# Kernel tuning notes

Hardware: AMD Instinct MI355X
Metric: run time of the kernel (lower is better)

The kernel has to match this reference:

```python
import jax, jax.numpy as jnp
import numpy as np

N_HEAD = 8
D_HEAD = 128   # dim_k = dim_q = dim_v
SEG_LEN = 512
EPS = 1e-6


def setup_inputs() -> dict:
    key = jax.random.key(0)
    ks = jax.random.split(key, 8)
    B, T, D = 2, 4096, 1024
    scale = 0.02
    x = jax.random.normal(ks[0], (B, T, D), dtype=jnp.float32)
    w_q = jax.random.normal(ks[1], (D, N_HEAD * D_HEAD), dtype=jnp.float32) * scale
    w_k = jax.random.normal(ks[2], (D, N_HEAD * D_HEAD), dtype=jnp.float32) * scale
    w_v = jax.random.normal(ks[3], (D, N_HEAD * D_HEAD), dtype=jnp.float32) * scale
    b_q = jnp.zeros((N_HEAD * D_HEAD,), jnp.float32)
    b_k = jnp.zeros((N_HEAD * D_HEAD,), jnp.float32)
    b_v = jnp.zeros((N_HEAD * D_HEAD,), jnp.float32)
    beta = jnp.zeros((N_HEAD,), jnp.float32)
    return {"x": x, "w_q": w_q, "b_q": b_q, "w_k": w_k, "b_k": b_k,
            "w_v": w_v, "b_v": b_v, "beta": beta}


def _heads(y, B, T):
    # [B,T,H*D] -> [B,H,T,D]
    return y.reshape(B, T, N_HEAD, D_HEAD).transpose(0, 2, 1, 3)


def reference(x, w_q, b_q, w_k, b_k, w_v, b_v, beta):
    B, T, _ = x.shape
    S = T // SEG_LEN
    q = _heads(x @ w_q + b_q, B, T)
    k = _heads(x @ w_k + b_k, B, T)
    v = _heads(x @ w_v + b_v, B, T)

    # segment: [B,H,T,D] -> [S,B,H,L,D]
    def seg(y):
        return y.reshape(B, N_HEAD, S, SEG_LEN, D_HEAD).transpose(2, 0, 1, 3, 4)
    qs, ks_, vs = seg(q), seg(k), seg(v)

    causal = jnp.tril(jnp.ones((SEG_LEN, SEG_LEN), bool))
    gate = jax.nn.sigmoid(beta).reshape(1, N_HEAD, 1, 1)
    inv_sqrt_d = 1.0 / jnp.sqrt(jnp.asarray(D_HEAD, x.dtype))

    def step(carry, segdat):
        M, z = carry                      # M: [B,H,Dk,Dv], z: [B,H,Dk]
        qc, kc, vc = segdat               # [B,H,L,D]
        sq = jax.nn.elu(qc) + 1.0
        sk = jax.nn.elu(kc) + 1.0
        # retrieval from memory BEFORE update
        a_mem = jnp.einsum('bhld,bhde->bhle', sq, M) / (
            jnp.einsum('bhld,bhd->bhl', sq, z)[..., None] + EPS)
        # delta-rule memory update
        retr_k = jnp.einsum('bhld,bhde->bhle', sk, M) / (
            jnp.einsum('bhld,bhd->bhl', sk, z)[..., None] + EPS)
        M = M + jnp.einsum('bhld,bhle->bhde', sk, vc - retr_k)
        z = z + sk.sum(axis=2)
        # local causal dot-product attention within the segment
        scores = jnp.einsum('bhld,bhmd->bhlm', qc, kc) * inv_sqrt_d
        scores = jnp.where(causal, scores, jnp.asarray(-1e30, scores.dtype))
        a_dot = jnp.einsum('bhlm,bhmd->bhld', jax.nn.softmax(scores, axis=-1), vc)
        # long-term context injection
        a = gate * a_mem + (1.0 - gate) * a_dot
        return (M, z), a

    M0 = jnp.zeros((B, N_HEAD, D_HEAD, D_HEAD), x.dtype)
    z0 = jnp.zeros((B, N_HEAD, D_HEAD), x.dtype)
    _, out = jax.lax.scan(step, (M0, z0), (qs, ks_, vs))
    # [S,B,H,L,D] -> [B,T,H*D]
    out = out.transpose(1, 3, 0, 2, 4).reshape(B, T, N_HEAD * D_HEAD)
    # wait: axes of out are [S,B,H,L,D]; reorder to [B,S,L,H,D]
    return out


# fix ordering: define reference properly (overrides above draft path)
def reference(x, w_q, b_q, w_k, b_k, w_v, b_v, beta):
    B, T, _ = x.shape
    S = T // SEG_LEN
    q = _heads(x @ w_q + b_q, B, T)
    k = _heads(x @ w_k + b_k, B, T)
    v = _heads(x @ w_v + b_v, B, T)

    def seg(y):
        return y.reshape(B, N_HEAD, S, SEG_LEN, D_HEAD).transpose(2, 0, 1, 3, 4)
    qs, ks_, vs = seg(q), seg(k), seg(v)

    causal = jnp.tril(jnp.ones((SEG_LEN, SEG_LEN), bool))
    gate = jax.nn.sigmoid(beta).reshape(1, N_HEAD, 1, 1)
    inv_sqrt_d = 1.0 / jnp.sqrt(jnp.asarray(D_HEAD, x.dtype))

    def step(carry, segdat):
        M, z = carry
        qc, kc, vc = segdat
        sq = jax.nn.elu(qc) + 1.0
        sk = jax.nn.elu(kc) + 1.0
        a_mem = jnp.einsum('bhld,bhde->bhle', sq, M) / (
            jnp.einsum('bhld,bhd->bhl', sq, z)[..., None] + EPS)
        retr_k = jnp.einsum('bhld,bhde->bhle', sk, M) / (
            jnp.einsum('bhld,bhd->bhl', sk, z)[..., None] + EPS)
        M = M + jnp.einsum('bhld,bhle->bhde', sk, vc - retr_k)
        z = z + sk.sum(axis=2)
        scores = jnp.einsum('bhld,bhmd->bhlm', qc, kc) * inv_sqrt_d
        scores = jnp.where(causal, scores, jnp.asarray(-1e30, scores.dtype))
        a_dot = jnp.einsum('bhlm,bhmd->bhld', jax.nn.softmax(scores, axis=-1), vc)
        a = gate * a_mem + (1.0 - gate) * a_dot
        return (M, z), a

    M0 = jnp.zeros((B, N_HEAD, D_HEAD, D_HEAD), x.dtype)
    z0 = jnp.zeros((B, N_HEAD, D_HEAD), x.dtype)
    _, out = jax.lax.scan(step, (M0, z0), (qs, ks_, vs))  # [S,B,H,L,D]
    out = out.transpose(1, 0, 3, 2, 4).reshape(B, T, N_HEAD * D_HEAD)
    return out
```

## Files before the change

### kernel.cpp

```cpp
#include <hip/hip_runtime.h>
#include <hip/hip_bf16.h>

typedef __attribute__((ext_vector_type(8))) short bf16x8;
typedef __attribute__((ext_vector_type(4))) float f32x4;
typedef unsigned short u16;
typedef unsigned int u32;

#define DEV static __device__ __forceinline__

DEV float bf2f(u16 u){ u32 x = ((u32)u)<<16; float f; __builtin_memcpy(&f,&x,4); return f; }
DEV u16 f2bf(float f){ u32 x; __builtin_memcpy(&x,&f,4); return (u16)((x + 0x7fffu + ((x>>16)&1u))>>16); }
DEV float elu1(float x){ return x > 0.f ? x + 1.f : __expf(x); }

DEV void gload16(const u16* g, u16* l){
  __builtin_amdgcn_global_load_lds(
      (const __attribute__((address_space(1))) unsigned int*)(g),
      (__attribute__((address_space(3))) unsigned int*)(l), 16, 0, 0);
}

#define MFMA(a,b,c) __builtin_amdgcn_mfma_f32_16x16x32_bf16((a),(b),(c),0,0,0)

#define NB 2
#define NT 4096
#define NH 8
#define DH 128
#define NS 8
#define SL 512
#define ND 1024
#define N3 3072
#define EPS 1e-6f

__global__ __launch_bounds__(256) void k_xc(const float* __restrict__ x, u16* __restrict__ xb){
  int i = blockIdx.x*256 + threadIdx.x;
  const float4 v0 = *(const float4*)(x + (size_t)i*8);
  const float4 v1 = *(const float4*)(x + (size_t)i*8 + 4);
  bf16x8 o;
  o[0]=(short)f2bf(v0.x); o[1]=(short)f2bf(v0.y); o[2]=(short)f2bf(v0.z); o[3]=(short)f2bf(v0.w);
  o[4]=(short)f2bf(v1.x); o[5]=(short)f2bf(v1.y); o[6]=(short)f2bf(v1.z); o[7]=(short)f2bf(v1.w);
  *(bf16x8*)(xb + (size_t)i*8) = o;
}

__global__ __launch_bounds__(256) void k_wt(const float* __restrict__ wq,
                                            const float* __restrict__ wk,
                                            const float* __restrict__ wv,
                                            u16* __restrict__ wt,
                                            float* __restrict__ cs){
  __shared__ float t[32][33];
  const int z = blockIdx.z;
  const float* w = (z==0) ? wq : (z==1 ? wk : wv);
  const int k0 = blockIdx.x*32, n0 = blockIdx.y*32;
  const int tx = threadIdx.x, ty = threadIdx.y;
  if (z==0 && blockIdx.x==0 && blockIdx.y==0){
    const int tid = ty*32 + tx;
#pragma unroll
    for (int i=0;i<64;i++) cs[tid + i*256] = 0.f;
  }
#pragma unroll
  for (int i=0;i<4;i++) t[ty+i*8][tx] = w[(size_t)(k0+ty+i*8)*ND + n0+tx];
  __syncthreads();
#pragma unroll
  for (int i=0;i<4;i++)
    wt[(size_t)(z*ND + n0+ty+i*8)*ND + k0+tx] = f2bf(t[tx][ty+i*8]);
}

__global__ __launch_bounds__(256) void k_gemm(const u16* __restrict__ xb,
                                              const u16* __restrict__ wt,
                                              const float* __restrict__ bq,
                                              const float* __restrict__ bk,
                                              const float* __restrict__ bv,
                                              u16* __restrict__ qkv){
  __shared__ __align__(16) u16 As[128*64];
  __shared__ __align__(16) u16 Bs[128*64];
  const int m0 = blockIdx.x*128, n0 = blockIdx.y*128;
  const int tid = threadIdx.x;
  const int w = tid>>6, lane = tid&63, g = lane>>4, li = lane&15;
  const int wr = w>>1, wc = w&1;
  const int srow = lane>>3;
  const int ssl  = (lane&7) ^ srow;
  f32x4 z4 = {0.f,0.f,0.f,0.f};
  f32x4 acc[4][4];
#pragma unroll
  for (int mi=0;mi<4;mi++)
#pragma unroll
    for (int ni=0;ni<4;ni++) acc[mi][ni] = z4;

  for (int kt=0; kt<16; ++kt){
    const int k0 = kt*64;
#pragma unroll
    for (int i=0;i<4;i++){
      const int c = i*4 + w;
      const int row = c*8 + srow;
      gload16(xb + (size_t)(m0+row)*ND + k0 + ssl*8, As + c*512);
      gload16(wt + (size_t)(n0+row)*ND + k0 + ssl*8, Bs + c*512);
    }
    __syncthreads();
#pragma unroll
    for (int kk=0;kk<2;kk++){
      bf16x8 a[4], bb[4];
#pragma unroll
      for (int mi=0;mi<4;mi++){
        int row = wr*64 + mi*16 + li;
        int slot = kk*4 + g;
        a[mi] = *(const bf16x8*)(As + row*64 + ((slot^(row&7))<<3));
      }
#pragma unroll
      for (int ni=0;ni<4;ni++){
        int row = wc*64 + ni*16 + li;
        int slot = kk*4 + g;
        bb[ni] = *(const bf16x8*)(Bs + row*64 + ((slot^(row&7))<<3));
      }
#pragma unroll
      for (int mi=0;mi<4;mi++)
#pragma unroll
        for (int ni=0;ni<4;ni++)
          acc[mi][ni] = MFMA(a[mi], bb[ni], acc[mi][ni]);
    }
    __syncthreads();
  }
#pragma unroll
  for (int ni=0;ni<4;ni++){
    int n = n0 + wc*64 + ni*16 + li;
    float bias = (n < ND) ? bq[n] : (n < 2*ND ? bk[n-ND] : bv[n-2*ND]);
#pragma unroll
    for (int mi=0;mi<4;mi++)
#pragma unroll
      for (int rr=0;rr<4;rr++){
        int m = m0 + wr*64 + mi*16 + 4*g + rr;
        qkv[(size_t)m*N3 + n] = f2bf(acc[mi][ni][rr] + bias);
      }
  }
}

__global__ __launch_bounds__(256) void k_tr(const u16* __restrict__ qkv,
                                            u16* __restrict__ vt,
                                            u16* __restrict__ pkT,
                                            float* __restrict__ cs){
  __shared__ __align__(4) u16 t[64*66];
  __shared__ float pf[8][64];
  const int t0 = blockIdx.x*64, d0 = blockIdx.y*64;
  const int z = blockIdx.z, bh = z>>1, part = z&1;
  const int b = bh>>3, h = bh&7;
  const int basec = (part ? 2*ND : ND) + h*DH;
  const int tid = threadIdx.x;
  float s0 = 0.f, s1 = 0.f;
#pragma unroll
  for (int i=0;i<8;i++){
    int fp = tid + i*256;
    int row = fp>>5, c2 = (fp&31)*2;
    ushort2 v = *(const ushort2*)(qkv + (size_t)(b*NT + t0+row)*N3 + basec + d0 + c2);
    if (!part){
      float e0 = elu1(bf2f(v.x)), e1 = elu1(bf2f(v.y));
      s0 += e0; s1 += e1;
      v.x = f2bf(e0); v.y = f2bf(e1);
    }
    *(ushort2*)(t + row*66 + c2) = v;
  }
  if (!part){ pf[tid>>5][(tid&31)*2] = s0; pf[tid>>5][(tid&31)*2+1] = s1; }
  __syncthreads();
  u16* dst = part ? vt : pkT;
#pragma unroll
  for (int i=0;i<8;i++){
    int fp = tid + i*256;
    int dr = fp>>5, c2 = (fp&31)*2;
    ushort2 v; v.x = t[c2*66 + dr]; v.y = t[(c2+1)*66 + dr];
    *(ushort2*)(dst + (size_t)(bh*DH + d0+dr)*NT + t0 + c2) = v;
  }
  if (!part && tid < 64){
    float a = 0.f;
#pragma unroll
    for (int r=0;r<8;r++) a += pf[r][tid];
    const int bhs = b*64 + h*8 + (t0>>9);
    atomicAdd(&cs[(size_t)bhs*DH + d0 + tid], a);
  }
}

__global__ __launch_bounds__(512) void k_dinv(const u16* __restrict__ qkv,
                                              const float* __restrict__ cs,
                                              float* __restrict__ dinvK){
  const int bhs = blockIdx.x, half = blockIdx.y;
  const int b = bhs>>6, h = (bhs>>3)&7, s = bhs&7;
  const int tid = threadIdx.x, w = tid>>6, lane = tid&63, grp = lane>>4, li = lane&15;
  __shared__ float zl[128];
  if (tid < 128){
    float a = 0.f;
    for (int sp=0; sp<s; ++sp) a += cs[(size_t)(bhs - s + sp)*DH + tid];
    zl[tid] = a;
  }
  __syncthreads();
#pragma unroll
  for (int it=0; it<8; ++it){
    const int r = half*256 + w*32 + it*4 + grp;
    bf16x8 v = *(const bf16x8*)(qkv + (size_t)(b*NT + s*SL + r)*N3 + ND + h*DH + li*8);
    float p = 0.f;
#pragma unroll
    for (int j=0;j<8;j++) p += elu1(bf2f((u16)v[j])) * zl[li*8+j];
    p += __shfl_xor(p,1); p += __shfl_xor(p,2);
    p += __shfl_xor(p,4); p += __shfl_xor(p,8);
    if (li == 0) dinvK[(size_t)bhs*SL + r] = 1.f/(p + EPS);
  }
}

__global__ __launch_bounds__(512) void k_gram(const u16* __restrict__ pkT,
                                              const u16* __restrict__ vtb,
                                              const float* __restrict__ dinvK,
                                              u16* __restrict__ G, float* __restrict__ Bm){
  const int bhs = blockIdx.x, ec = blockIdx.y;
  const int bh = bhs>>3, s = bhs&7, tb = s*SL;
  const int tid = threadIdx.x, w = tid>>6, lane = tid&63, g = lane>>4, li = lane&15;
  __shared__ __align__(16) u16 Bk[32*512];
  __shared__ __align__(16) u16 Bv[32*512];
  __shared__ float dv[512];
  dv[tid] = dinvK[(size_t)bhs*SL + tid];
#pragma unroll
  for (int i=0;i<4;i++){
    const int ee = i*8 + w;
    const size_t rowo = ((size_t)bh*DH + ec*32 + ee)*NT + tb + ((lane^w)<<3);
    gload16(pkT + rowo, Bk + ee*512);
    gload16(vtb + rowo, Bv + ee*512);
  }
  __syncthreads();
  f32x4 z4 = {0.f,0.f,0.f,0.f};
  f32x4 Ga[2] = {z4,z4}, Ba[2] = {z4,z4};
  const u16* arow = pkT + ((size_t)bh*DH + 16*w + li)*NT + tb;
  for (int ks=0; ks<16; ++ks){
    const int r0 = ks*32 + g*8;
    bf16x8 araw = *(const bf16x8*)(arow + r0);
    float4 d0 = *(const float4*)(dv + r0);
    float4 d1 = *(const float4*)(dv + r0 + 4);
    bf16x8 ascl;
    ascl[0] = (short)f2bf(bf2f((u16)araw[0]) * d0.x);
    ascl[1] = (short)f2bf(bf2f((u16)araw[1]) * d0.y);
    ascl[2] = (short)f2bf(bf2f((u16)araw[2]) * d0.z);
    ascl[3] = (short)f2bf(bf2f((u16)araw[3]) * d0.w);
    ascl[4] = (short)f2bf(bf2f((u16)araw[4]) * d1.x);
    ascl[5] = (short)f2bf(bf2f((u16)araw[5]) * d1.y);
    ascl[6] = (short)f2bf(bf2f((u16)araw[6]) * d1.z);
    ascl[7] = (short)f2bf(bf2f((u16)araw[7]) * d1.w);
    const int slot = ks*4 + g;
#pragma unroll
    for (int ni=0;ni<2;ni++){
      const int ee = ni*16 + li;
      bf16x8 bk8 = *(const bf16x8*)(Bk + ee*512 + ((slot^(li&7))<<3));
      bf16x8 bv8 = *(const bf16x8*)(Bv + ee*512 + ((slot^(li&7))<<3));
      Ga[ni] = MFMA(ascl, bk8, Ga[ni]);
      Ba[ni] = MFMA(araw, bv8, Ba[ni]);
    }
  }
#pragma unroll
  for (int ni=0;ni<2;ni++)
#pragma unroll
    for (int rr=0;rr<4;rr++){
      const int dd = 16*w + 4*g + rr;
      const int ee = ec*32 + ni*16 + li;
      G[((size_t)bhs*DH + dd)*DH + ee] = f2bf(Ga[ni][rr]);
      Bm[((size_t)bhs*DH + dd)*DH + ee] = Ba[ni][rr];
    }
}

__global__ __launch_bounds__(512) void k_scan(const u16* __restrict__ G,
                                              const float* __restrict__ Bm,
                                              u16* __restrict__ MTs){
  const int bh = blockIdx.x;
  const int tid = threadIdx.x, w = tid>>6, lane = tid&63, g = lane>>4, li = lane&15;
  __shared__ __align__(16) u16 MT[16384];
  for (int i = tid; i < 16384; i += 512) MT[i] = 0;
  __syncthreads();
  for (int s=0;s<NS;s++){
    const size_t bhs = (size_t)bh*NS + s;
    for (int f = tid; f < 2048; f += 512){
      int e = f>>4, sl = f&15;
      bf16x8 v = *(const bf16x8*)(MT + e*128 + ((sl^(e&7))<<3));
      *(bf16x8*)(MTs + bhs*16384 + e*128 + sl*8) = v;
    }
    __syncthreads();
    f32x4 z4 = {0.f,0.f,0.f,0.f};
    f32x4 acc[8];
#pragma unroll
    for (int i=0;i<8;i++) acc[i] = z4;
#pragma unroll
    for (int ks=0;ks<4;ks++){
      bf16x8 a = *(const bf16x8*)(G + (bhs*DH + 16*w + li)*DH + ks*32 + g*8);
#pragma unroll
      for (int ni=0;ni<8;ni++){
        int e = ni*16 + li;
        int sl = ks*4 + g;
        bf16x8 bfr = *(const bf16x8*)(MT + e*128 + ((sl^(e&7))<<3));
        acc[ni] = MFMA(a, bfr, acc[ni]);
      }
    }
    __syncthreads();
#pragma unroll
    for (int ni=0;ni<8;ni++)
#pragma unroll
      for (int rr=0;rr<4;rr++){
        int dd = 16*w + 4*g + rr, ee = ni*16 + li;
        float delta = Bm[(bhs*DH + dd)*DH + ee] - acc[ni][rr];
        int idx = ee*128 + (((dd>>3)^(ee&7))<<3) + (dd&7);
        MT[idx] = f2bf(bf2f(MT[idx]) + delta);
      }
    __syncthreads();
  }
}

__global__ __launch_bounds__(512) void k_attn(const u16* __restrict__ qkv,
                                              const u16* __restrict__ vtb,
                                              const u16* __restrict__ MTs,
                                              const float* __restrict__ cs,
                                              const float* __restrict__ beta,
                                              float* __restrict__ out){
  const int bhs = blockIdx.x, half = blockIdx.y;
  const int b = bhs>>6, h = (bhs>>3)&7, s = bhs&7, bh = bhs>>3;
  const int tid = threadIdx.x, w = tid>>6, lane = tid&63, g = lane>>4, li = lane&15;
  const int jq = (w < 4) ? (half + 2*w) : (15 - half - 2*(w-4));
  const int qb = jq*32;
  const float gate = 1.f/(1.f + __expf(-beta[h]));
  const float isd = 0.08838834764831845f;
  const float L2E = 1.4426950408889634f;
  __shared__ __align__(16) u16 P[8*1024];
  __shared__ float zl[128];
  __shared__ float dinvW[8][32];
  u16* Pw = P + w*1024;

  if (tid < 128){
    float a = 0.f;
    for (int sp=0; sp<s; ++sp) a += cs[(size_t)(bhs - s + sp)*DH + tid];
    zl[tid] = a;
  }
  __syncthreads();

  {
    const int r = qb + (lane&31);
    const int dh = (lane>>5)*64;
    const u16* qrow = qkv + (size_t)(b*NT + s*SL + r)*N3 + h*DH + dh;
    float p = 0.f;
#pragma unroll
    for (int j=0;j<64;j+=8){
      bf16x8 v = *(const bf16x8*)(qrow + j);
#pragma unroll
      for (int t=0;t<8;t++) p += elu1(bf2f((u16)v[t])) * zl[dh + j + t];
    }
    p += __shfl_xor(p, 32);
    if (lane < 32) dinvW[w][lane] = 1.f/(p + EPS);
  }

  bf16x8 qf[2][4];
#pragma unroll
  for (int mf=0; mf<2; ++mf)
#pragma unroll
    for (int kf=0; kf<4; ++kf)
      qf[mf][kf] = *(const bf16x8*)(qkv + (size_t)(b*NT + s*SL + qb + mf*16 + li)*N3 + h*DH + kf*32 + g*8);

  f32x4 z4 = {0.f,0.f,0.f,0.f};
  f32x4 O[2][8];
  float mr[2][4], lr[2][4];
#pragma unroll
  for (int mf=0;mf<2;++mf){
#pragma unroll
    for (int nf=0;nf<8;++nf) O[mf][nf] = z4;
#pragma unroll
    for (int rr=0;rr<4;++rr){ mr[mf][rr] = -3e38f; lr[mf][rr] = 0.f; }
  }

  const int nch = jq + 1;
  for (int c=0; c<nch; ++c){
    const int kb = c*32;
    f32x4 sa[2][2];
#pragma unroll
    for (int mf=0;mf<2;++mf)
#pragma unroll
      for (int nf=0;nf<2;++nf) sa[mf][nf] = z4;
#pragma unroll
    for (int kf=0; kf<4; ++kf)
#pragma unroll
      for (int nf=0; nf<2; ++nf){
        bf16x8 bk8 = *(const bf16x8*)(qkv + (size_t)(b*NT + s*SL + kb + nf*16 + li)*N3 + ND + h*DH + kf*32 + g*8);
        sa[0][nf] = MFMA(qf[0][kf], bk8, sa[0][nf]);
        sa[1][nf] = MFMA(qf[1][kf], bk8, sa[1][nf]);
      }
    float pv[2][2][4];
#pragma unroll
    for (int mf=0;mf<2;++mf)
#pragma unroll
      for (int nf=0;nf<2;++nf)
#pragma unroll
        for (int rr=0;rr<4;++rr){
          int row = qb + mf*16 + 4*g + rr, col = kb + nf*16 + li;
          float v = sa[mf][nf][rr]*isd;
          pv[mf][nf][rr] = (col > row) ? -1e30f : v;
        }
#pragma unroll
    for (int mf=0;mf<2;++mf)
#pragma unroll
      for (int rr=0;rr<4;++rr){
        float cm = fmaxf(pv[mf][0][rr], pv[mf][1][rr]);
        cm = fmaxf(cm, __shfl_xor(cm, 1));
        cm = fmaxf(cm, __shfl_xor(cm, 2));
        cm = fmaxf(cm, __shfl_xor(cm, 4));
        cm = fmaxf(cm, __shfl_xor(cm, 8));
        float mo = mr[mf][rr];
        float mn = fmaxf(mo, cm);
        float sc = exp2f((mo - mn)*L2E);
        float rs = 0.f;
#pragma unroll
        for (int nf=0;nf<2;++nf){
          float p = exp2f((pv[mf][nf][rr]-mn)*L2E);
          pv[mf][nf][rr] = p; rs += p;
        }
        rs += __shfl_xor(rs, 1); rs += __shfl_xor(rs, 2);
        rs += __shfl_xor(rs, 4); rs += __shfl_xor(rs, 8);
        lr[mf][rr] = lr[mf][rr]*sc + rs;
        mr[mf][rr] = mn;
#pragma unroll
        for (int nf=0;nf<8;++nf) O[mf][nf][rr] *= sc;
      }
#pragma unroll
    for (int mf=0;mf<2;++mf)
#pragma unroll
      for (int nf=0;nf<2;++nf)
#pragma unroll
        for (int rr=0;rr<4;++rr){
          int row = mf*16 + 4*g + rr, col = nf*16 + li;
          Pw[row*32 + (((col>>3)^(row&3))<<3) + (col&7)] = f2bf(pv[mf][nf][rr]);
        }
    bf16x8 pa[2];
#pragma unroll
    for (int mf=0;mf<2;++mf){
      int row = mf*16 + li;
      pa[mf] = *(const bf16x8*)(Pw + row*32 + ((g^(row&3))<<3));
    }
#pragma unroll
    for (int nf=0;nf<8;++nf){
      bf16x8 bv8 = *(const bf16x8*)(vtb + ((size_t)bh*DH + nf*16 + li)*NT + s*SL + kb + g*8);
      O[0][nf] = MFMA(pa[0], bv8, O[0][nf]);
      O[1][nf] = MFMA(pa[1], bv8, O[1][nf]);
    }
  }

  f32x4 Am[2][8];
#pragma unroll
  for (int mf=0;mf<2;++mf)
#pragma unroll
    for (int nf=0;nf<8;++nf) Am[mf][nf] = z4;
#pragma unroll
  for (int ks=0;ks<4;++ks){
    bf16x8 pq[2];
#pragma unroll
    for (int mf=0;mf<2;++mf){
      bf16x8 raw = *(const bf16x8*)(qkv + (size_t)(b*NT + s*SL + qb + mf*16 + li)*N3 + h*DH + ks*32 + g*8);
#pragma unroll
      for (int j=0;j<8;j++) raw[j] = (short)f2bf(elu1(bf2f((u16)raw[j])));
      pq[mf] = raw;
    }
#pragma unroll
    for (int nf=0;nf<8;++nf){
      bf16x8 bfr = *(const bf16x8*)(MTs + ((size_t)bhs*DH + nf*16 + li)*DH + ks*32 + g*8);
      Am[0][nf] = MFMA(pq[0], bfr, Am[0][nf]);
      Am[1][nf] = MFMA(pq[1], bfr, Am[1][nf]);
    }
  }

  const float og = 1.f - gate;
#pragma unroll
  for (int mf=0;mf<2;++mf)
#pragma unroll
    for (int rr=0;rr<4;++rr){
      int row = qb + mf*16 + 4*g + rr;
      float invd = og / lr[mf][rr];
      float dv = gate * dinvW[w][row - qb];
#pragma unroll
      for (int nf=0;nf<8;++nf)
        out[(size_t)(b*NT + s*SL + row)*ND + h*DH + nf*16 + li] =
            O[mf][nf][rr]*invd + Am[mf][nf][rr]*dv;
    }
}

extern "C" void kernel_launch(void* const* d_in, const int* in_sizes, int n_in,
                              void* d_out, int out_size, void* d_ws, size_t ws_size,
                              hipStream_t stream) {
  (void)in_sizes; (void)n_in; (void)out_size; (void)ws_size;
  const float* x    = (const float*)d_in[0];
  const float* wq   = (const float*)d_in[1];
  const float* bq   = (const float*)d_in[2];
  const float* wk   = (const float*)d_in[3];
  const float* bk   = (const float*)d_in[4];
  const float* wv   = (const float*)d_in[5];
  const float* bv   = (const float*)d_in[6];
  const float* beta = (const float*)d_in[7];
  float* out = (float*)d_out;
  char* ws = (char*)d_ws;

  u16*   wt  = (u16*)  (ws + 0);
  u16*   qkv = (u16*)  (ws + 6291456);
  u16*   vt  = (u16*)  (ws + 56623104);
  u16*   pkT = (u16*)  (ws + 73400320);
  u16*   G   = (u16*)  (ws + 90177536);
  float* Bm  = (float*)(ws + 94371840);
  u16*   MTs = (u16*)  (ws + 102760448);
  float* cs  = (float*)(ws + 106954752);
  u16*   xb  = vt;
  float* dinvK = (float*)(ws + 107020288);

  hipLaunchKernelGGL(k_xc,    dim3(4096),    dim3(256),  0, stream, x, xb);
  hipLaunchKernelGGL(k_wt,    dim3(32,32,3), dim3(32,8), 0, stream, wq, wk, wv, wt, cs);
  hipLaunchKernelGGL(k_gemm,  dim3(64,24),   dim3(256),  0, stream, xb, wt, bq, bk, bv, qkv);
  hipLaunchKernelGGL(k_tr,    dim3(64,2,32), dim3(256),  0, stream, qkv, vt, pkT, cs);
  hipLaunchKernelGGL(k_dinv,  dim3(128,2),   dim3(512),  0, stream, qkv, cs, dinvK);
  hipLaunchKernelGGL(k_gram,  dim3(128,4),   dim3(512),  0, stream, pkT, vt, dinvK, G, Bm);
  hipLaunchKernelGGL(k_scan,  dim3(16),      dim3(512),  0, stream, G, Bm, MTs);
  hipLaunchKernelGGL(k_attn,  dim3(128,2),   dim3(512),  0, stream, qkv, vt, MTs, cs, beta, out);
}
```

Baseline: 203.8 us.

## Double-buffer QKV GEMM with 256x256 tiles and phased async prefetch

Rewrites the bf16 QKV projection GEMM to use 256x256 block tiles with 512 threads and double-buffered LDS. The next k-tile is prefetched in four slices spread across four compute phases, with explicit vmcnt waits, barriers and raised MFMA issue priority. The goal is to hide global-to-LDS load latency behind MFMA work and to reuse each LDS tile more. In exchange, the 128KB LDS footprint allows only one block per CU, and 384 blocks on the CUs leave a partial second wave.

```diff
diff --git a/kernel.cpp b/kernel.cpp
--- a/kernel.cpp
+++ b/kernel.cpp
@@ -63,70 +63,116 @@
     wt[(size_t)(z*ND + n0+ty+i*8)*ND + k0+tx] = f2bf(t[tx][ty+i*8]);
 }
 
-__global__ __launch_bounds__(256) void k_gemm(const u16* __restrict__ xb,
+__global__ __launch_bounds__(512) void k_gemm(const u16* __restrict__ xb,
                                               const u16* __restrict__ wt,
                                               const float* __restrict__ bq,
                                               const float* __restrict__ bk,
                                               const float* __restrict__ bv,
                                               u16* __restrict__ qkv){
-  __shared__ __align__(16) u16 As[128*64];
-  __shared__ __align__(16) u16 Bs[128*64];
-  const int m0 = blockIdx.x*128, n0 = blockIdx.y*128;
-  const int tid = threadIdx.x;
-  const int w = tid>>6, lane = tid&63, g = lane>>4, li = lane&15;
-  const int wr = w>>1, wc = w&1;
+  __shared__ __align__(16) u16 As[2][256*64];
+  __shared__ __align__(16) u16 Bs[2][256*64];
+  const int tid = threadIdx.x, w = tid>>6, lane = tid&63, g = lane>>4, li = lane&15;
+  const int wr = w>>2, wc = w&3;
+  const int m0 = blockIdx.x*256, n0 = blockIdx.y*256;
   const int srow = lane>>3;
   const int ssl  = (lane&7) ^ srow;
+
   f32x4 z4 = {0.f,0.f,0.f,0.f};
-  f32x4 acc[4][4];
-#pragma unroll
-  for (int mi=0;mi<4;mi++)
-#pragma unroll
-    for (int ni=0;ni<4;ni++) acc[mi][ni] = z4;
-
-  for (int kt=0; kt<16; ++kt){
-    const int k0 = kt*64;
-#pragma unroll
-    for (int i=0;i<4;i++){
-      const int c = i*4 + w;
-      const int row = c*8 + srow;
-      gload16(xb + (size_t)(m0+row)*ND + k0 + ssl*8, As + c*512);
-      gload16(wt + (size_t)(n0+row)*ND + k0 + ssl*8, Bs + c*512);
-    }
-    __syncthreads();
-#pragma unroll
-    for (int kk=0;kk<2;kk++){
-      bf16x8 a[4], bb[4];
-#pragma unroll
-      for (int mi=0;mi<4;mi++){
-        int row = wr*64 + mi*16 + li;
-        int slot = kk*4 + g;
-        a[mi] = *(const bf16x8*)(As + row*64 + ((slot^(row&7))<<3));
+  f32x4 acc[8][4];
+#pragma unroll
+  for (int mi=0;mi<8;mi++)
+#pragma unroll
+    for (int nf=0;nf<4;nf++) acc[mi][nf] = z4;
+
+#define STG(t_, h_) do{                                                         \
+    u16* dst_ = ((h_)&1) ? (u16*)Bs[(t_)&1] : (u16*)As[(t_)&1];                 \
+    const u16* src_ = ((h_)&1) ? wt : xb;                                       \
+    const int o0_ = ((h_)&1) ? n0 : m0;                                         \
+    const int rb0_ = (((h_)>>1)<<7) + w*8;                                      \
+    _Pragma("unroll")                                                           \
+    for (int r_=0;r_<2;r_++){                                                   \
+      const int rb_ = rb0_ + r_*64;                                             \
+      gload16(src_ + (size_t)(o0_+rb_+srow)*ND + (t_)*64 + ssl*8, dst_ + rb_*64);\
+    }                                                                           \
+  }while(0)
+
+#define PHASE(q_) do{                                                           \
+    if (t<15) STG(t+1, q_);                                                     \
+    bf16x8 a_[2][2];                                                            \
+    _Pragma("unroll")                                                           \
+    for (int m2_=0;m2_<2;m2_++)                                                 \
+    _Pragma("unroll")                                                           \
+    for (int kk_=0;kk_<2;kk_++){                                                \
+      const int row_ = wr*128 + ((q_)*2+m2_)*16 + li;                           \
+      a_[m2_][kk_] = *(const bf16x8*)(Ab + row_*64 + (((kk_*4+g)^(row_&7))<<3));\
+    }                                                                           \
+    __builtin_amdgcn_s_setprio(1);                                              \
+    _Pragma("unroll")                                                           \
+    for (int kk_=0;kk_<2;kk_++)                                                 \
+    _Pragma("unroll")                                                           \
+    for (int m2_=0;m2_<2;m2_++)                                                 \
+    _Pragma("unroll")                                                           \
+    for (int nf_=0;nf_<4;nf_++)                                                 \
+      acc[(q_)*2+m2_][nf_] = MFMA(a_[m2_][kk_], bfv[nf_][kk_], acc[(q_)*2+m2_][nf_]); \
+    __builtin_amdgcn_s_setprio(0);                                              \
+    __builtin_amdgcn_s_barrier();                                               \
+    __builtin_amdgcn_sched_barrier(0);                                          \
+  }while(0)
+
+  STG(0,0); STG(0,1); STG(0,2); STG(0,3);
+  for (int t=0; t<16; ++t){
+    const u16* Ab = (const u16*)As[t&1];
+    const u16* Bb = (const u16*)Bs[t&1];
+    if (t<15){ STG(t+1,0); asm volatile("s_waitcnt vmcnt(2)" ::: "memory"); }
+    else     {             asm volatile("s_waitcnt vmcnt(0)" ::: "memory"); }
+    __builtin_amdgcn_s_barrier();
+    __builtin_amdgcn_sched_barrier(0);
+    bf16x8 bfv[4][2];
+#pragma unroll
+    for (int nf=0;nf<4;nf++)
+#pragma unroll
+      for (int kk=0;kk<2;kk++){
+        const int row = wc*64 + nf*16 + li;
+        bfv[nf][kk] = *(const bf16x8*)(Bb + row*64 + (((kk*4+g)^(row&7))<<3));
       }
-#pragma unroll
-      for (int ni=0;ni<4;ni++){
-        int row = wc*64 + ni*16 + li;
-        int slot = kk*4 + g;
-        bb[ni] = *(const bf16x8*)(Bs + row*64 + ((slot^(row&7))<<3));
-      }
-#pragma unroll
-      for (int mi=0;mi<4;mi++)
-#pragma unroll
-        for (int ni=0;ni<4;ni++)
-          acc[mi][ni] = MFMA(a[mi], bb[ni], acc[mi][ni]);
-    }
-    __syncthreads();
-  }
-#pragma unroll
-  for (int ni=0;ni<4;ni++){
-    int n = n0 + wc*64 + ni*16 + li;
-    float bias = (n < ND) ? bq[n] : (n < 2*ND ? bk[n-ND] : bv[n-2*ND]);
-#pragma unroll
-    for (int mi=0;mi<4;mi++)
+    {
+      bf16x8 a_[2][2];
+#pragma unroll
+      for (int m2=0;m2<2;m2++)
+#pragma unroll
+        for (int kk=0;kk<2;kk++){
+          const int row = wr*128 + m2*16 + li;
+          a_[m2][kk] = *(const bf16x8*)(Ab + row*64 + (((kk*4+g)^(row&7))<<3));
+        }
+      __builtin_amdgcn_s_setprio(1);
+#pragma unroll
+      for (int kk=0;kk<2;kk++)
+#pragma unroll
+        for (int m2=0;m2<2;m2++)
+#pragma unroll
+          for (int nf=0;nf<4;nf++)
+            acc[m2][nf] = MFMA(a_[m2][kk], bfv[nf][kk], acc[m2][nf]);
+      __builtin_amdgcn_s_setprio(0);
+      __builtin_amdgcn_s_barrier();
+      __builtin_amdgcn_sched_barrier(0);
+    }
+    PHASE(1);
+    PHASE(2);
+    PHASE(3);
+  }
+#undef PHASE
+#undef STG
+
+#pragma unroll
+  for (int nf=0;nf<4;nf++){
+    const int n = n0 + wc*64 + nf*16 + li;
+    const float bias = (n < ND) ? bq[n] : (n < 2*ND ? bk[n-ND] : bv[n-2*ND]);
+#pragma unroll
+    for (int mi=0;mi<8;mi++)
 #pragma unroll
       for (int rr=0;rr<4;rr++){
-        int m = m0 + wr*64 + mi*16 + 4*g + rr;
-        qkv[(size_t)m*N3 + n] = f2bf(acc[mi][ni][rr] + bias);
+        const int m = m0 + wr*128 + mi*16 + 4*g + rr;
+        qkv[(size_t)m*N3 + n] = f2bf(acc[mi][nf][rr] + bias);
       }
   }
 }
@@ -502,7 +548,7 @@
 
   hipLaunchKernelGGL(k_xc,    dim3(4096),    dim3(256),  0, stream, x, xb);
   hipLaunchKernelGGL(k_wt,    dim3(32,32,3), dim3(32,8), 0, stream, wq, wk, wv, wt, cs);
-  hipLaunchKernelGGL(k_gemm,  dim3(64,24),   dim3(256),  0, stream, xb, wt, bq, bk, bv, qkv);
+  hipLaunchKernelGGL(k_gemm,  dim3(32,12),   dim3(512),  0, stream, xb, wt, bq, bk, bv, qkv);
   hipLaunchKernelGGL(k_tr,    dim3(64,2,32), dim3(256),  0, stream, qkv, vt, pkT, cs);
   hipLaunchKernelGGL(k_dinv,  dim3(128,2),   dim3(512),  0, stream, qkv, cs, dinvK);
   hipLaunchKernelGGL(k_gram,  dim3(128,4),   dim3(512),  0, stream, pkT, vt, dinvK, G, Bm);
```

New measurement: 238.5 us. 17.0% more time.
